# Optimization experiments

Hardware: AMD Instinct MI355X
Metric: run time of the kernel (lower is better)

Reference implementation:

```python
import jax, jax.numpy as jnp
import numpy as np

KERNEL_MUL = 2.0
KERNEL_NUM = 5


def setup_inputs() -> dict:
    key = jax.random.key(0)
    k1, k2 = jax.random.split(key)
    n, d = 4096, 256
    source = jax.random.normal(k1, (n, d), dtype=jnp.float32)
    target = jax.random.normal(k2, (n, d), dtype=jnp.float32) + 0.5  # slight domain shift
    return {"source": source, "target": target}


def _gaussian_kernel_sum(source, target):
    # total: (2n, d)
    total = jnp.concatenate([source, target], axis=0)
    n_samples = total.shape[0]
    # Pairwise squared L2 via x^2 + y^2 - 2xy (same math as the (2n,2n,d) broadcast)
    sq = jnp.sum(total * total, axis=1)  # (2n,)
    l2 = sq[:, None] + sq[None, :] - 2.0 * (total @ total.T)  # (2n, 2n)
    l2 = jnp.maximum(l2, 0.0)
    # bandwidth from detached distances (torch uses L2_distance.data)
    bandwidth = jax.lax.stop_gradient(jnp.sum(l2)) / (n_samples ** 2 - n_samples)
    bandwidth = bandwidth / (KERNEL_MUL ** (KERNEL_NUM // 2))
    # sum of multi-bandwidth RBF kernels
    kernels = jnp.zeros_like(l2)
    for i in range(KERNEL_NUM):
        kernels = kernels + jnp.exp(-l2 / (bandwidth * (KERNEL_MUL ** i)))
    return kernels


def reference(source, target):
    b = source.shape[0]
    kernels = _gaussian_kernel_sum(source, target)
    xx = jnp.mean(kernels[:b, :b])
    yy = jnp.mean(kernels[b:, b:])
    xy = jnp.mean(kernels[:b, b:])
    yx = jnp.mean(kernels[b:, :b])
    return xx + yy - xy - yx
```

## Files before the change

kernel.cpp:

```cpp
#include <hip/hip_runtime.h>

#define N_TOT 8192
#define NB    4096
#define DDIM  256
#define NTILE 64
#define NBLK  (NTILE * (NTILE + 1) / 2)
#define PREP_BLKS 256

#define WAITCNT_VM8 3960
#define WAITCNT_VM0 3952

typedef __bf16 bf16x8 __attribute__((ext_vector_type(8)));
typedef float  f32x4  __attribute__((ext_vector_type(4)));
typedef float  f32x2  __attribute__((ext_vector_type(2)));

__device__ inline unsigned short f2bf_rne(float x) {
    unsigned int u = __float_as_uint(x);
    unsigned int r = (u + 0x7fffu + ((u >> 16) & 1u)) >> 16;
    return (unsigned short)r;
}

__device__ inline void gl2lds16(const unsigned short* g, unsigned short* ldsbase) {
    __builtin_amdgcn_global_load_lds(
        (const __attribute__((address_space(1))) unsigned int*)g,
        (__attribute__((address_space(3))) unsigned int*)ldsbase, 16, 0, 0);
}


__global__ __launch_bounds__(128) void prep(const float* __restrict__ src,
                                            const float* __restrict__ tgt,
                                            float* __restrict__ sq,
                                            unsigned short* __restrict__ totp,
                                            float* __restrict__ colp) {
    __shared__ unsigned short pbuf[2][32 * 136];
    __shared__ float cs[2 * 256];
    int t = threadIdx.x, w = t >> 6, lane = t & 63;
    int panel = blockIdx.x * 2 + w;
    int row0  = panel * 16;

    float4 csum = {0.f, 0.f, 0.f, 0.f};
    int ls_base = (lane >> 1) * 136 + (lane & 1) * 4;
    #pragma unroll
    for (int r = 0; r < 16; ++r) {
        int row = row0 + r;
        const float* rp = (row < NB) ? (src + (size_t)row * DDIM)
                                     : (tgt + (size_t)(row - NB) * DDIM);
        float4 v = ((const float4*)rp)[lane];
        ushort4 o;
        o.x = f2bf_rne(v.x); o.y = f2bf_rne(v.y);
        o.z = f2bf_rne(v.z); o.w = f2bf_rne(v.w);
        *(ushort4*)&pbuf[w][ls_base + r * 8] = o;
        float s = v.x*v.x + v.y*v.y + v.z*v.z + v.w*v.w;
        #pragma unroll
        for (int off = 32; off > 0; off >>= 1) s += __shfl_down(s, off);
        if (lane == 0) sq[row] = s;
        csum.x += v.x; csum.y += v.y; csum.z += v.z; csum.w += v.w;
    }
    #pragma unroll
    for (int it = 0; it < 16; ++it) {
        int g  = it * 256 + lane * 4;
        int kq = g >> 7, wi = g & 127;
        ushort4 o = *(const ushort4*)&pbuf[w][kq * 136 + wi];
        *(ushort4*)(totp + (size_t)panel * 4096 + g) = o;
    }
    cs[w * 256 + lane * 4 + 0] = csum.x;
    cs[w * 256 + lane * 4 + 1] = csum.y;
    cs[w * 256 + lane * 4 + 2] = csum.z;
    cs[w * 256 + lane * 4 + 3] = csum.w;
    __syncthreads();
    colp[blockIdx.x * 256 + t]       = cs[t] + cs[256 + t];
    colp[blockIdx.x * 256 + t + 128] = cs[t + 128] + cs[256 + t + 128];
}

__global__ void finalize_bw(const float* __restrict__ colp,
                            const float* __restrict__ sq,
                            float* __restrict__ wsf) {
    __shared__ float redA[4], redB[4];
    int t = threadIdx.x, lane = t & 63, w = t >> 6;
    float a[8];
    #pragma unroll
    for (int u = 0; u < 8; ++u) a[u] = 0.f;
    for (int b = 0; b < PREP_BLKS; b += 8) {
        #pragma unroll
        for (int u = 0; u < 8; ++u) a[u] += colp[(b + u) * 256 + t];
    }
    float sv = ((a[0] + a[1]) + (a[2] + a[3])) + ((a[4] + a[5]) + (a[6] + a[7]));
    float s8[8];
    #pragma unroll
    for (int u = 0; u < 8; ++u) s8[u] = 0.f;
    for (int i = 0; i < 32; i += 8) {
        #pragma unroll
        for (int u = 0; u < 8; ++u) s8[u] += sq[(i + u) * 256 + t];
    }
    float s1 = ((s8[0] + s8[1]) + (s8[2] + s8[3])) + ((s8[4] + s8[5]) + (s8[6] + s8[7]));
    float v2 = sv * sv;
    #pragma unroll
    for (int off = 32; off > 0; off >>= 1) {
        s1 += __shfl_down(s1, off);
        v2 += __shfl_down(v2, off);
    }
    if (lane == 0) { redA[w] = s1; redB[w] = v2; }
    __syncthreads();
    if (t == 0) {
        float S1   = redA[0] + redA[1] + redA[2] + redA[3];
        float sdot = redB[0] + redB[1] + redB[2] + redB[3];
        float bw_sum = 2.0f * (float)N_TOT * S1 - 2.0f * sdot;
        double denom = (double)N_TOT * (double)N_TOT - (double)N_TOT;
        float bandwidth = (float)((double)bw_sum / denom) * 0.25f;
        wsf[2] = (1.0f / bandwidth) * 0.0625f * 1.44269504f;
    }
}

__global__ __launch_bounds__(256) void mmd_tiles(const unsigned short* __restrict__ totp,
                                                 const float* __restrict__ sq,
                                                 const float* __restrict__ wsf,
                                                 float* __restrict__ part) {
    __shared__ unsigned short ringA[4][2][4][512];
    __shared__ unsigned short ringB[4][2][4][512];
    __shared__ float redf[4];

    int idx = blockIdx.x;
    int ti = (int)((129.0f - sqrtf(16641.0f - 8.0f * (float)idx)) * 0.5f);
    if (ti > 63) ti = 63;
    if (ti < 0)  ti = 0;
    while ((ti * (129 - ti)) / 2 > idx) --ti;
    while (((ti + 1) * (128 - ti)) / 2 <= idx) ++ti;
    int tj = ti + idx - (ti * (129 - ti)) / 2;

    int t = threadIdx.x;
    int wid = t >> 6, lane = t & 63;
    int rl = lane & 15, q = lane >> 4;
    int gi0 = ti * 128, gj0 = tj * 128;
    int ia = (wid >> 1) * 64, jb = (wid & 1) * 64;

    float c = wsf[2];

    f32x4 sqi4[4];
    float sqjv[4];
    #pragma unroll
    for (int m = 0; m < 4; ++m)
        sqi4[m] = *(const f32x4*)(sq + gi0 + ia + m * 16 + q * 4);
    #pragma unroll
    for (int n = 0; n < 4; ++n)
        sqjv[n] = sq[gj0 + jb + n * 16 + rl];
    __builtin_amdgcn_s_waitcnt(WAITCNT_VM0);

    const unsigned short* pa[4];
    const unsigned short* pb[4];
    int pA0 = (gi0 + ia) >> 4, pB0 = (gj0 + jb) >> 4;
    #pragma unroll
    for (int m = 0; m < 4; ++m) {
        pa[m] = totp + (size_t)(pA0 + m) * 4096 + lane * 8;
        pb[m] = totp + (size_t)(pB0 + m) * 4096 + lane * 8;
    }

    f32x4 acc[4][4];
    #pragma unroll
    for (int m = 0; m < 4; ++m)
        #pragma unroll
        for (int n = 0; n < 4; ++n) acc[m][n] = (f32x4){0.f, 0.f, 0.f, 0.f};

    #pragma unroll
    for (int m = 0; m < 4; ++m) {
        gl2lds16(pa[m], &ringA[wid][0][m][0]);
        gl2lds16(pb[m], &ringB[wid][0][m][0]);
    }
    #pragma unroll
    for (int m = 0; m < 4; ++m) {
        gl2lds16(pa[m] + 512, &ringA[wid][1][m][0]);
        gl2lds16(pb[m] + 512, &ringB[wid][1][m][0]);
    }

    #pragma unroll
    for (int s = 0; s < 8; ++s) {
        const int slot = s & 1;
        if (s < 7) __builtin_amdgcn_s_waitcnt(WAITCNT_VM8);
        else       __builtin_amdgcn_s_waitcnt(WAITCNT_VM0);
        bf16x8 av[4], bv[4];
        #pragma unroll
        for (int m = 0; m < 4; ++m)
            av[m] = *(const bf16x8*)&ringA[wid][slot][m][lane * 8];
        #pragma unroll
        for (int n = 0; n < 4; ++n)
            bv[n] = *(const bf16x8*)&ringB[wid][slot][n][lane * 8];
        #pragma unroll
        for (int m = 0; m < 4; ++m)
            #pragma unroll
            for (int n = 0; n < 4; ++n)
                acc[m][n] = __builtin_amdgcn_mfma_f32_16x16x32_bf16(av[m], bv[n], acc[m][n], 0, 0, 0);
        if (s < 6) {
            const int so = (s + 2) * 512;
            #pragma unroll
            for (int m = 0; m < 4; ++m) {
                gl2lds16(pa[m] + so, &ringA[wid][slot][m][0]);
                gl2lds16(pb[m] + so, &ringB[wid][slot][m][0]);
            }
        }
    }

    float tc = 2.0f * c;
    f32x2 lsum = {0.f, 0.f};
    #pragma unroll
    for (int m = 0; m < 4; ++m) {
        f32x4 ai;
        ai[0] = sqi4[m][0] * c; ai[1] = sqi4[m][1] * c;
        ai[2] = sqi4[m][2] * c; ai[3] = sqi4[m][3] * c;
        #pragma unroll
        for (int n = 0; n < 4; ++n) {
            float bj = sqjv[n] * c;
            #pragma unroll
            for (int ep = 0; ep < 2; ++ep) {
                f32x2 x;
                x[0] = __builtin_fmaf(acc[m][n][2*ep+0], tc, -(ai[2*ep+0] + bj));
                x[1] = __builtin_fmaf(acc[m][n][2*ep+1], tc, -(ai[2*ep+1] + bj));
                f32x2 E;
                E[0] = __builtin_amdgcn_exp2f(x[0]);
                E[1] = __builtin_amdgcn_exp2f(x[1]);
                f32x2 E2 = E * E, E4 = E2 * E2, E8 = E4 * E4;
                lsum += ((E + E2) + (E4 + E8)) + E8 * E8;
            }
        }
    }
    float local = lsum[0] + lsum[1];
    #pragma unroll
    for (int off = 32; off > 0; off >>= 1) local += __shfl_down(local, off);
    if (lane == 0) redf[wid] = local;
    __syncthreads();
    if (t == 0) {
        float tot = redf[0] + redf[1] + redf[2] + redf[3];
        float scale = (((ti < 32) == (tj < 32)) ? 1.0f : -1.0f) * ((ti == tj) ? 1.0f : 2.0f);
        part[idx] = tot * scale;
    }
}

__global__ void write_out(const float* __restrict__ part, float* __restrict__ out) {
    __shared__ float red[4];
    int t = threadIdx.x, lane = t & 63, w = t >> 6;
    float s = 0.f;
    for (int i = t; i < NBLK; i += 256) s += part[i];
    #pragma unroll
    for (int off = 32; off > 0; off >>= 1) s += __shfl_down(s, off);
    if (lane == 0) red[w] = s;
    __syncthreads();
    if (t == 0)
        out[0] = (red[0] + red[1] + red[2] + red[3]) * (1.0f / ((float)NB * (float)NB));
}

extern "C" void kernel_launch(void* const* d_in, const int* in_sizes, int n_in,
                              void* d_out, int out_size, void* d_ws, size_t ws_size,
                              hipStream_t stream) {
    const float* src = (const float*)d_in[0];
    const float* tgt = (const float*)d_in[1];
    float* wsf  = (float*)d_ws;
    float* sq   = wsf + 512;
    float* part = wsf + 16384;
    float* colp = wsf + 32768;
    unsigned short* totp = (unsigned short*)((char*)d_ws + 524288);

    prep<<<PREP_BLKS, 128, 0, stream>>>(src, tgt, sq, totp, colp);
    finalize_bw<<<1, 256, 0, stream>>>(colp, sq, wsf);
    mmd_tiles<<<NBLK, 256, 0, stream>>>(totp, sq, wsf, part);
    write_out<<<1, 256, 0, stream>>>(part, (float*)d_out);
}
```

Baseline: 110.2 us.

## Load MFMA operands directly to registers and process two tiles per block

Replaces the global-to-LDS async ring buffer with direct global loads into registers, double-buffered across k-steps. The grid is halved so each block loops over two triangular tiles, resetting the reduction each time. This removes LDS staging and manual waitcnt handling, but it gives up the asynchronous prefetch depth and raises register pressure. Having fewer blocks may also hurt load balance across CUs.

```diff
diff --git a/kernel.cpp b/kernel.cpp
--- a/kernel.cpp
+++ b/kernel.cpp
@@ -5,10 +5,8 @@
 #define DDIM  256
 #define NTILE 64
 #define NBLK  (NTILE * (NTILE + 1) / 2)
+#define PGRID (NBLK / 2)
 #define PREP_BLKS 256
-
-#define WAITCNT_VM8 3960
-#define WAITCNT_VM0 3952
 
 typedef __bf16 bf16x8 __attribute__((ext_vector_type(8)));
 typedef float  f32x4  __attribute__((ext_vector_type(4)));
@@ -18,12 +16,6 @@
     unsigned int u = __float_as_uint(x);
     unsigned int r = (u + 0x7fffu + ((u >> 16) & 1u)) >> 16;
     return (unsigned short)r;
-}
-
-__device__ inline void gl2lds16(const unsigned short* g, unsigned short* ldsbase) {
-    __builtin_amdgcn_global_load_lds(
-        (const __attribute__((address_space(1))) unsigned int*)g,
-        (__attribute__((address_space(3))) unsigned int*)ldsbase, 16, 0, 0);
 }
 
 
@@ -115,121 +107,109 @@
                                                  const float* __restrict__ sq,
                                                  const float* __restrict__ wsf,
                                                  float* __restrict__ part) {
-    __shared__ unsigned short ringA[4][2][4][512];
-    __shared__ unsigned short ringB[4][2][4][512];
     __shared__ float redf[4];
-
-    int idx = blockIdx.x;
-    int ti = (int)((129.0f - sqrtf(16641.0f - 8.0f * (float)idx)) * 0.5f);
-    if (ti > 63) ti = 63;
-    if (ti < 0)  ti = 0;
-    while ((ti * (129 - ti)) / 2 > idx) --ti;
-    while (((ti + 1) * (128 - ti)) / 2 <= idx) ++ti;
-    int tj = ti + idx - (ti * (129 - ti)) / 2;
 
     int t = threadIdx.x;
     int wid = t >> 6, lane = t & 63;
     int rl = lane & 15, q = lane >> 4;
-    int gi0 = ti * 128, gj0 = tj * 128;
-    int ia = (wid >> 1) * 64, jb = (wid & 1) * 64;
-
-    float c = wsf[2];
-
-    f32x4 sqi4[4];
-    float sqjv[4];
-    #pragma unroll
-    for (int m = 0; m < 4; ++m)
-        sqi4[m] = *(const f32x4*)(sq + gi0 + ia + m * 16 + q * 4);
-    #pragma unroll
-    for (int n = 0; n < 4; ++n)
-        sqjv[n] = sq[gj0 + jb + n * 16 + rl];
-    __builtin_amdgcn_s_waitcnt(WAITCNT_VM0);
-
-    const unsigned short* pa[4];
-    const unsigned short* pb[4];
-    int pA0 = (gi0 + ia) >> 4, pB0 = (gj0 + jb) >> 4;
-    #pragma unroll
-    for (int m = 0; m < 4; ++m) {
-        pa[m] = totp + (size_t)(pA0 + m) * 4096 + lane * 8;
-        pb[m] = totp + (size_t)(pB0 + m) * 4096 + lane * 8;
-    }
-
-    f32x4 acc[4][4];
-    #pragma unroll
-    for (int m = 0; m < 4; ++m)
-        #pragma unroll
-        for (int n = 0; n < 4; ++n) acc[m][n] = (f32x4){0.f, 0.f, 0.f, 0.f};
-
-    #pragma unroll
-    for (int m = 0; m < 4; ++m) {
-        gl2lds16(pa[m], &ringA[wid][0][m][0]);
-        gl2lds16(pb[m], &ringB[wid][0][m][0]);
-    }
-    #pragma unroll
-    for (int m = 0; m < 4; ++m) {
-        gl2lds16(pa[m] + 512, &ringA[wid][1][m][0]);
-        gl2lds16(pb[m] + 512, &ringB[wid][1][m][0]);
-    }
-
-    #pragma unroll
-    for (int s = 0; s < 8; ++s) {
-        const int slot = s & 1;
-        if (s < 7) __builtin_amdgcn_s_waitcnt(WAITCNT_VM8);
-        else       __builtin_amdgcn_s_waitcnt(WAITCNT_VM0);
-        bf16x8 av[4], bv[4];
+    float c  = wsf[2];
+    float tc = 2.0f * c;
+
+    #pragma unroll 1
+    for (int r = 0; r < 2; ++r) {
+        int idx = blockIdx.x + r * PGRID;
+
+        int ti = (int)((129.0f - sqrtf(16641.0f - 8.0f * (float)idx)) * 0.5f);
+        if (ti > 63) ti = 63;
+        if (ti < 0)  ti = 0;
+        while ((ti * (129 - ti)) / 2 > idx) --ti;
+        while (((ti + 1) * (128 - ti)) / 2 <= idx) ++ti;
+        int tj = ti + idx - (ti * (129 - ti)) / 2;
+
+        int gi0 = ti * 128, gj0 = tj * 128;
+        int ia = (wid >> 1) * 64, jb = (wid & 1) * 64;
+
+        f32x4 sqi4[4];
+        float sqjv[4];
         #pragma unroll
         for (int m = 0; m < 4; ++m)
-            av[m] = *(const bf16x8*)&ringA[wid][slot][m][lane * 8];
+            sqi4[m] = *(const f32x4*)(sq + gi0 + ia + m * 16 + q * 4);
         #pragma unroll
         for (int n = 0; n < 4; ++n)
-            bv[n] = *(const bf16x8*)&ringB[wid][slot][n][lane * 8];
+            sqjv[n] = sq[gj0 + jb + n * 16 + rl];
+
+        const unsigned short* pa[4];
+        const unsigned short* pb[4];
+        int pA0 = (gi0 + ia) >> 4, pB0 = (gj0 + jb) >> 4;
+        #pragma unroll
+        for (int m = 0; m < 4; ++m) {
+            pa[m] = totp + (size_t)(pA0 + m) * 4096 + lane * 8;
+            pb[m] = totp + (size_t)(pB0 + m) * 4096 + lane * 8;
+        }
+
+        f32x4 acc[4][4];
         #pragma unroll
         for (int m = 0; m < 4; ++m)
             #pragma unroll
-            for (int n = 0; n < 4; ++n)
-                acc[m][n] = __builtin_amdgcn_mfma_f32_16x16x32_bf16(av[m], bv[n], acc[m][n], 0, 0, 0);
-        if (s < 6) {
-            const int so = (s + 2) * 512;
+            for (int n = 0; n < 4; ++n) acc[m][n] = (f32x4){0.f, 0.f, 0.f, 0.f};
+
+        bf16x8 av[2][4], bv[2][4];
+        #pragma unroll
+        for (int m = 0; m < 4; ++m) {
+            av[0][m] = *(const bf16x8*)(pa[m]);
+            bv[0][m] = *(const bf16x8*)(pb[m]);
+        }
+        #pragma unroll
+        for (int s = 0; s < 8; ++s) {
+            const int cur = s & 1, nxt = cur ^ 1;
+            if (s < 7) {
+                const int so = (s + 1) * 512;
+                #pragma unroll
+                for (int m = 0; m < 4; ++m) {
+                    av[nxt][m] = *(const bf16x8*)(pa[m] + so);
+                    bv[nxt][m] = *(const bf16x8*)(pb[m] + so);
+                }
+            }
             #pragma unroll
-            for (int m = 0; m < 4; ++m) {
-                gl2lds16(pa[m] + so, &ringA[wid][slot][m][0]);
-                gl2lds16(pb[m] + so, &ringB[wid][slot][m][0]);
+            for (int m = 0; m < 4; ++m)
+                #pragma unroll
+                for (int n = 0; n < 4; ++n)
+                    acc[m][n] = __builtin_amdgcn_mfma_f32_16x16x32_bf16(av[cur][m], bv[cur][n], acc[m][n], 0, 0, 0);
+        }
+
+        f32x2 lsum = {0.f, 0.f};
+        #pragma unroll
+        for (int m = 0; m < 4; ++m) {
+            f32x4 ai;
+            ai[0] = sqi4[m][0] * c; ai[1] = sqi4[m][1] * c;
+            ai[2] = sqi4[m][2] * c; ai[3] = sqi4[m][3] * c;
+            #pragma unroll
+            for (int n = 0; n < 4; ++n) {
+                float bj = sqjv[n] * c;
+                #pragma unroll
+                for (int ep = 0; ep < 2; ++ep) {
+                    f32x2 x;
+                    x[0] = __builtin_fmaf(acc[m][n][2*ep+0], tc, -(ai[2*ep+0] + bj));
+                    x[1] = __builtin_fmaf(acc[m][n][2*ep+1], tc, -(ai[2*ep+1] + bj));
+                    f32x2 E;
+                    E[0] = __builtin_amdgcn_exp2f(x[0]);
+                    E[1] = __builtin_amdgcn_exp2f(x[1]);
+                    f32x2 E2 = E * E, E4 = E2 * E2, E8 = E4 * E4;
+                    lsum += ((E + E2) + (E4 + E8)) + E8 * E8;
+                }
             }
         }
-    }
-
-    float tc = 2.0f * c;
-    f32x2 lsum = {0.f, 0.f};
-    #pragma unroll
-    for (int m = 0; m < 4; ++m) {
-        f32x4 ai;
-        ai[0] = sqi4[m][0] * c; ai[1] = sqi4[m][1] * c;
-        ai[2] = sqi4[m][2] * c; ai[3] = sqi4[m][3] * c;
-        #pragma unroll
-        for (int n = 0; n < 4; ++n) {
-            float bj = sqjv[n] * c;
-            #pragma unroll
-            for (int ep = 0; ep < 2; ++ep) {
-                f32x2 x;
-                x[0] = __builtin_fmaf(acc[m][n][2*ep+0], tc, -(ai[2*ep+0] + bj));
-                x[1] = __builtin_fmaf(acc[m][n][2*ep+1], tc, -(ai[2*ep+1] + bj));
-                f32x2 E;
-                E[0] = __builtin_amdgcn_exp2f(x[0]);
-                E[1] = __builtin_amdgcn_exp2f(x[1]);
-                f32x2 E2 = E * E, E4 = E2 * E2, E8 = E4 * E4;
-                lsum += ((E + E2) + (E4 + E8)) + E8 * E8;
-            }
-        }
-    }
-    float local = lsum[0] + lsum[1];
-    #pragma unroll
-    for (int off = 32; off > 0; off >>= 1) local += __shfl_down(local, off);
-    if (lane == 0) redf[wid] = local;
-    __syncthreads();
-    if (t == 0) {
-        float tot = redf[0] + redf[1] + redf[2] + redf[3];
-        float scale = (((ti < 32) == (tj < 32)) ? 1.0f : -1.0f) * ((ti == tj) ? 1.0f : 2.0f);
-        part[idx] = tot * scale;
+        float local = lsum[0] + lsum[1];
+        #pragma unroll
+        for (int off = 32; off > 0; off >>= 1) local += __shfl_down(local, off);
+        if (lane == 0) redf[wid] = local;
+        __syncthreads();
+        if (t == 0) {
+            float tot = redf[0] + redf[1] + redf[2] + redf[3];
+            float scale = (((ti < 32) == (tj < 32)) ? 1.0f : -1.0f) * ((ti == tj) ? 1.0f : 2.0f);
+            part[idx] = tot * scale;
+        }
+        __syncthreads();
     }
 }
 
@@ -259,6 +239,6 @@
 
     prep<<<PREP_BLKS, 128, 0, stream>>>(src, tgt, sq, totp, colp);
     finalize_bw<<<1, 256, 0, stream>>>(colp, sq, wsf);
-    mmd_tiles<<<NBLK, 256, 0, stream>>>(totp, sq, wsf, part);
+    mmd_tiles<<<PGRID, 256, 0, stream>>>(totp, sq, wsf, part);
     write_out<<<1, 256, 0, stream>>>(part, (float*)d_out);
 }
```

Result: slower. 114.4 us (+3.8%).
